# Optimization experiments

Hardware: AMD Instinct MI355X
Metric: run time of the kernel (lower is better)

The kernel has to match this reference:

```python
import jax, jax.numpy as jnp
import numpy as np

M, K, N = 32768, 2048, 2048  # tokens, in_features, out_features
QMIN, QMAX = -128, 127


def setup_inputs() -> dict:
    key = jax.random.key(0)
    ks = jax.random.split(key, 7)
    x = jax.random.normal(ks[0], (M, K), dtype=jnp.float32).astype(jnp.float16)
    int_weight = jax.random.randint(ks[1], (N, K), QMIN, QMAX + 1, dtype=jnp.int32).astype(jnp.int8)
    # calibrated-looking asymmetric activation quant params (fp16 buffers, [num_steps]=1)
    act_delta = (jax.random.uniform(ks[2], (1,), dtype=jnp.float32) * 0.02 + 0.005).astype(jnp.float16)
    act_zp = jnp.round(jax.random.normal(ks[3], (1,), dtype=jnp.float32) * 8.0).astype(jnp.float16)
    # per-output-channel weight scales; fuse precomputed dequant buffers consistently
    w_delta = jax.random.uniform(ks[4], (N,), dtype=jnp.float32) * 0.002 + 1e-4
    act_times_weight_delta = (act_delta.astype(jnp.float32) * w_delta)[None, :]  # [1, N]
    w_row_sum = jnp.sum(int_weight.astype(jnp.float32), axis=1)  # [N]
    zp_times_weight_channel_sum = (act_zp.astype(jnp.float32) * w_row_sum * act_times_weight_delta[0])[None, :]  # [1, N]
    bias = jax.random.normal(ks[5], (N,), dtype=jnp.float32) * 0.02
    return {
        "input": x,
        "act_delta": act_delta,
        "act_zp": act_zp,
        "zp_times_weight_channel_sum": zp_times_weight_channel_sum,
        "act_times_weight_delta": act_times_weight_delta,
        "bias": bias,
        "int_weight": int_weight,
    }


def reference(input, act_delta, act_zp, zp_times_weight_channel_sum,
              act_times_weight_delta, bias, int_weight):
    # current_step == num_steps - 1 == 0
    delta = act_delta[0].astype(jnp.float32)
    zp = act_zp[0].astype(jnp.float32)
    atwd = act_times_weight_delta[0]            # [N] = act_delta * weight_delta
    zp_sum = zp_times_weight_channel_sum[0]     # [N] = zp * rowsum(W_int) * atwd
    # asymmetric int8 activation quantization: q = clip(round(x/delta + zp))
    q = jnp.clip(jnp.round(input.astype(jnp.float32) / delta + zp), QMIN, QMAX).astype(jnp.int8)
    # int8 GEMM with int32 accumulation: [M,K] x [K,N]
    acc = jnp.matmul(q.astype(jnp.int32), int_weight.astype(jnp.int32).T)
    # fused dequant + zero-point correction + bias, cast to fp16
    out = acc.astype(jnp.float32) * atwd - zp_sum + bias
    return out.astype(jnp.float16)
```

## Files before the change

kernel.cpp:

```cpp
#include <hip/hip_runtime.h>
#include <hip/hip_fp16.h>
#include <stdint.h>

typedef int i32x4 __attribute__((ext_vector_type(4)));

#define BM 256
#define BN 256
#define BKB 64
#define NSLOT 4
#define SLOT_BYTES 32768
#define THREADS 512

__device__ __forceinline__ void gload_lds16(const void* g, void* l) {
  __builtin_amdgcn_global_load_lds(
      (const __attribute__((address_space(1))) unsigned int*)g,
      (__attribute__((address_space(3))) unsigned int*)l, 16, 0, 0);
}

__global__ __launch_bounds__(256) void quant_x_kernel(
    const float* __restrict__ x, const float* __restrict__ deltap,
    const float* __restrict__ zpp, int8_t* __restrict__ q, int n16) {
  int i = blockIdx.x * blockDim.x + threadIdx.x;
  if (i >= n16) return;
  const float rdelta = 1.0f / deltap[0];
  const float zp = zpp[0];
  const float4* src = (const float4*)x + (size_t)i * 4;
  int packed[4];
#pragma unroll
  for (int g = 0; g < 4; ++g) {
    float4 v = src[g];
    float f0 = fminf(127.f, fmaxf(-128.f, rintf(fmaf(v.x, rdelta, zp))));
    float f1 = fminf(127.f, fmaxf(-128.f, rintf(fmaf(v.y, rdelta, zp))));
    float f2 = fminf(127.f, fmaxf(-128.f, rintf(fmaf(v.z, rdelta, zp))));
    float f3 = fminf(127.f, fmaxf(-128.f, rintf(fmaf(v.w, rdelta, zp))));
    int q0 = (int)f0 & 255, q1 = (int)f1 & 255, q2 = (int)f2 & 255, q3 = (int)f3 & 255;
    packed[g] = q0 | (q1 << 8) | (q2 << 16) | (q3 << 24);
  }
  ((int4*)q)[i] = make_int4(packed[0], packed[1], packed[2], packed[3]);
}

__global__ __launch_bounds__(256) void pack_w_kernel(
    const int* __restrict__ w, int8_t* __restrict__ wp, int n16) {
  int i = blockIdx.x * blockDim.x + threadIdx.x;
  if (i >= n16) return;
  const int4* src = (const int4*)w + (size_t)i * 4;
  int packed[4];
#pragma unroll
  for (int g = 0; g < 4; ++g) {
    int4 v = src[g];
    packed[g] = (v.x & 255) | ((v.y & 255) << 8) | ((v.z & 255) << 16) | ((v.w & 255) << 24);
  }
  ((int4*)wp)[i] = make_int4(packed[0], packed[1], packed[2], packed[3]);
}

__global__ __launch_bounds__(THREADS, 2) void gemm_i8_kernel(
    const int8_t* __restrict__ Aq, const int8_t* __restrict__ Bw,
    const float* __restrict__ atwd, const float* __restrict__ zpws,
    const float* __restrict__ bias, float* __restrict__ out,
    int Mc, int Nc, int Kc) {
  __shared__ int8_t lds[NSLOT * SLOT_BYTES];

  const int nwg = gridDim.x;
  int bid = blockIdx.x;
  if ((nwg & 7) == 0) bid = (bid & 7) * (nwg >> 3) + (bid >> 3);
  const int nbn = Nc / BN;
  const int bm = bid / nbn;
  const int bn = bid % nbn;

  const int tid = threadIdx.x;
  const size_t K = (size_t)Kc;
  const int NT = Kc / BKB;

  const int srow = tid >> 2;
  const int c_log = (tid & 3) ^ ((tid >> 3) & 3);
  const int8_t* gA = Aq + ((size_t)(bm * BM + srow)) * K + c_log * 16;
  const int8_t* gB = Bw + ((size_t)(bn * BN + srow)) * K + c_log * 16;
  const size_t half_off = (size_t)128 * K;
  int8_t* ldst = &lds[tid * 16];

  auto stageA = [&](int t, int h) {
    gload_lds16(gA + (size_t)h * half_off + (size_t)t * BKB,
                ldst + (t & 3) * SLOT_BYTES + h * 8192);
  };
  auto stageB = [&](int t, int h) {
    gload_lds16(gB + (size_t)h * half_off + (size_t)t * BKB,
                ldst + (t & 3) * SLOT_BYTES + 16384 + h * 8192);
  };

  const int lane = tid & 63;
  const int wave = tid >> 6;
  const int wr = wave >> 2;
  const int wc = wave & 3;
  const int fr = lane & 15;
  const int kc = lane >> 4;
  const int coff = (kc ^ ((fr >> 1) & 3)) << 4;
  const int aRow = wr * 128 + fr;
  const int bRow = wc * 64 + fr;

  i32x4 acc[8][4] = {};

  stageA(0, 0); stageA(0, 1); stageB(0, 0); stageB(0, 1);
  if (NT > 1) { stageA(1, 0); stageA(1, 1); stageB(1, 0); stageB(1, 1); }
  if (NT > 2) { stageA(2, 0); stageA(2, 1); stageB(2, 0); stageB(2, 1); }
  if (NT >= 3) asm volatile("s_waitcnt vmcnt(8)" ::: "memory");
  else         asm volatile("s_waitcnt vmcnt(0)" ::: "memory");
  __builtin_amdgcn_s_barrier();

  for (int t = 0; t < NT; ++t) {
    const int8_t* sA = &lds[(t & 3) * SLOT_BYTES];
    const int8_t* sB = sA + 16384;
    const bool pf = (t + 3 < NT);
    i32x4 bfr[4], afr[4];

#pragma unroll
    for (int j = 0; j < 4; ++j)
      bfr[j] = *(const i32x4*)&sB[(bRow + j * 16) * 64 + coff];
#pragma unroll
    for (int i = 0; i < 4; ++i)
      afr[i] = *(const i32x4*)&sA[(aRow + i * 16) * 64 + coff];
    if (pf) { stageA(t + 3, 0); stageA(t + 3, 1); }
    __builtin_amdgcn_s_barrier();
    asm volatile("s_waitcnt lgkmcnt(0)" ::: "memory");
    __builtin_amdgcn_s_setprio(1);
#pragma unroll
    for (int i = 0; i < 4; ++i)
#pragma unroll
      for (int j = 0; j < 4; ++j)
        acc[i][j] = __builtin_amdgcn_mfma_i32_16x16x64_i8(afr[i], bfr[j], acc[i][j], 0, 0, 0);
    __builtin_amdgcn_s_setprio(0);
    __builtin_amdgcn_s_barrier();

#pragma unroll
    for (int i = 0; i < 4; ++i)
      afr[i] = *(const i32x4*)&sA[(aRow + 64 + i * 16) * 64 + coff];
    if (pf) { stageB(t + 3, 0); stageB(t + 3, 1); }
    __builtin_amdgcn_s_barrier();
    asm volatile("s_waitcnt lgkmcnt(0)" ::: "memory");
    __builtin_amdgcn_s_setprio(1);
#pragma unroll
    for (int i = 0; i < 4; ++i)
#pragma unroll
      for (int j = 0; j < 4; ++j)
        acc[4 + i][j] = __builtin_amdgcn_mfma_i32_16x16x64_i8(afr[i], bfr[j], acc[4 + i][j], 0, 0, 0);
    __builtin_amdgcn_s_setprio(0);
    if (t < NT - 3)       asm volatile("s_waitcnt vmcnt(8)" ::: "memory");
    else if (t == NT - 3) asm volatile("s_waitcnt vmcnt(4)" ::: "memory");
    else if (t == NT - 2) asm volatile("s_waitcnt vmcnt(0)" ::: "memory");
    __builtin_amdgcn_s_barrier();
  }

  const int r4 = (lane >> 4) << 2;
#pragma unroll
  for (int j = 0; j < 4; ++j) {
    const int cn = bn * BN + wc * 64 + j * 16 + fr;
    const float aw = atwd[cn];
    const float zs = zpws[cn];
    const float bs = bias[cn];
#pragma unroll
    for (int mi = 0; mi < 8; ++mi) {
      const size_t rbase = (size_t)(bm * BM + wr * 128 + mi * 16 + r4) * (size_t)Nc;
#pragma unroll
      for (int r = 0; r < 4; ++r) {
        float v = (float)acc[mi][j][r] * aw - zs + bs;
        v = __half2float(__float2half(v));
        out[rbase + (size_t)r * Nc + cn] = v;
      }
    }
  }
}

extern "C" void kernel_launch(void* const* d_in, const int* in_sizes, int n_in,
                              void* d_out, int out_size, void* d_ws, size_t ws_size,
                              hipStream_t stream) {
  const float* x         = (const float*)d_in[0];
  const float* act_delta = (const float*)d_in[1];
  const float* act_zp    = (const float*)d_in[2];
  const float* zpws      = (const float*)d_in[3];
  const float* atwd      = (const float*)d_in[4];
  const float* bias      = (const float*)d_in[5];
  const int*   w32       = (const int*)d_in[6];
  float* out = (float*)d_out;

  const int N = in_sizes[5];
  const int K = in_sizes[6] / N;
  const int M = in_sizes[0] / K;

  int8_t* q  = (int8_t*)d_ws;
  int8_t* wp = q + (size_t)M * K;

  {
    int n16 = (M * K) / 16;
    quant_x_kernel<<<(n16 + 255) / 256, 256, 0, stream>>>(x, act_delta, act_zp, q, n16);
  }
  {
    int n16 = (N * K) / 16;
    pack_w_kernel<<<(n16 + 255) / 256, 256, 0, stream>>>(w32, wp, n16);
  }
  {
    dim3 grid((M / BM) * (N / BN));
    gemm_i8_kernel<<<grid, THREADS, 0, stream>>>(q, wp, atwd, zpws, bias, out, M, N, K);
  }
}
```

Before: 271.1 us.

## Switch GEMM to BK=128 double-buffered LDS pipeline and grid-stride quantizer

Restructures the int8 GEMM main loop from a 4-slot, BK=64 ring with a prefetch depth of three tiles into a 2-slot, BK=128 double buffer. Each 64-wide K half of the next tile is prefetched in pieces interleaved with the four MFMA phases. This halves the number of outer iterations and amortizes barriers over more MFMA work, but prefetches only one tile ahead, so global-load latency may be less well hidden. The activation quantization kernel also becomes a grid-stride loop capped at 2048 blocks, which cuts block launch overhead.

```diff
diff --git a/kernel.cpp b/kernel.cpp
--- a/kernel.cpp
+++ b/kernel.cpp
@@ -6,10 +6,9 @@
 
 #define BM 256
 #define BN 256
-#define BKB 64
-#define NSLOT 4
-#define SLOT_BYTES 32768
+#define BK 128
 #define THREADS 512
+#define SLOT 65536
 
 __device__ __forceinline__ void gload_lds16(const void* g, void* l) {
   __builtin_amdgcn_global_load_lds(
@@ -20,23 +19,24 @@
 __global__ __launch_bounds__(256) void quant_x_kernel(
     const float* __restrict__ x, const float* __restrict__ deltap,
     const float* __restrict__ zpp, int8_t* __restrict__ q, int n16) {
-  int i = blockIdx.x * blockDim.x + threadIdx.x;
-  if (i >= n16) return;
   const float rdelta = 1.0f / deltap[0];
   const float zp = zpp[0];
-  const float4* src = (const float4*)x + (size_t)i * 4;
-  int packed[4];
-#pragma unroll
-  for (int g = 0; g < 4; ++g) {
-    float4 v = src[g];
-    float f0 = fminf(127.f, fmaxf(-128.f, rintf(fmaf(v.x, rdelta, zp))));
-    float f1 = fminf(127.f, fmaxf(-128.f, rintf(fmaf(v.y, rdelta, zp))));
-    float f2 = fminf(127.f, fmaxf(-128.f, rintf(fmaf(v.z, rdelta, zp))));
-    float f3 = fminf(127.f, fmaxf(-128.f, rintf(fmaf(v.w, rdelta, zp))));
-    int q0 = (int)f0 & 255, q1 = (int)f1 & 255, q2 = (int)f2 & 255, q3 = (int)f3 & 255;
-    packed[g] = q0 | (q1 << 8) | (q2 << 16) | (q3 << 24);
-  }
-  ((int4*)q)[i] = make_int4(packed[0], packed[1], packed[2], packed[3]);
+  for (int i = blockIdx.x * blockDim.x + threadIdx.x; i < n16;
+       i += gridDim.x * blockDim.x) {
+    const float4* src = (const float4*)x + (size_t)i * 4;
+    int packed[4];
+#pragma unroll
+    for (int g = 0; g < 4; ++g) {
+      float4 v = src[g];
+      float f0 = fminf(127.f, fmaxf(-128.f, rintf(fmaf(v.x, rdelta, zp))));
+      float f1 = fminf(127.f, fmaxf(-128.f, rintf(fmaf(v.y, rdelta, zp))));
+      float f2 = fminf(127.f, fmaxf(-128.f, rintf(fmaf(v.z, rdelta, zp))));
+      float f3 = fminf(127.f, fmaxf(-128.f, rintf(fmaf(v.w, rdelta, zp))));
+      int q0 = (int)f0 & 255, q1 = (int)f1 & 255, q2 = (int)f2 & 255, q3 = (int)f3 & 255;
+      packed[g] = q0 | (q1 << 8) | (q2 << 16) | (q3 << 24);
+    }
+    ((int4*)q)[i] = make_int4(packed[0], packed[1], packed[2], packed[3]);
+  }
 }
 
 __global__ __launch_bounds__(256) void pack_w_kernel(
@@ -58,7 +58,7 @@
     const float* __restrict__ atwd, const float* __restrict__ zpws,
     const float* __restrict__ bias, float* __restrict__ out,
     int Mc, int Nc, int Kc) {
-  __shared__ int8_t lds[NSLOT * SLOT_BYTES];
+  __shared__ int8_t lds[2 * SLOT];
 
   const int nwg = gridDim.x;
   int bid = blockIdx.x;
@@ -69,22 +69,21 @@
 
   const int tid = threadIdx.x;
   const size_t K = (size_t)Kc;
-  const int NT = Kc / BKB;
+  const int NT = Kc / BK;
 
   const int srow = tid >> 2;
-  const int c_log = (tid & 3) ^ ((tid >> 3) & 3);
-  const int8_t* gA = Aq + ((size_t)(bm * BM + srow)) * K + c_log * 16;
-  const int8_t* gB = Bw + ((size_t)(bn * BN + srow)) * K + c_log * 16;
-  const size_t half_off = (size_t)128 * K;
-  int8_t* ldst = &lds[tid * 16];
-
-  auto stageA = [&](int t, int h) {
-    gload_lds16(gA + (size_t)h * half_off + (size_t)t * BKB,
-                ldst + (t & 3) * SLOT_BYTES + h * 8192);
-  };
-  auto stageB = [&](int t, int h) {
-    gload_lds16(gB + (size_t)h * half_off + (size_t)t * BKB,
-                ldst + (t & 3) * SLOT_BYTES + 16384 + h * 8192);
+  const int lc = (tid & 3) ^ ((tid >> 3) & 3);
+  const int8_t* gA = Aq + ((size_t)(bm * BM + srow)) * K + lc * 16;
+  const int8_t* gB = Bw + ((size_t)(bn * BN + srow)) * K + lc * 16;
+  int8_t* lbase = &lds[tid * 16];
+  const size_t row128 = (size_t)128 * K;
+
+  auto stage = [&](int tt, int kh, int ab) {
+    const int8_t* g = ab ? gB : gA;
+    int8_t* l = lbase + (tt & 1) * SLOT + ab * 32768 + kh * 16384;
+    const size_t koff = (size_t)tt * BK + (size_t)kh * 64;
+    gload_lds16(g + koff, l);
+    gload_lds16(g + koff + row128, l + 8192);
   };
 
   const int lane = tid & 63;
@@ -93,60 +92,65 @@
   const int wc = wave & 3;
   const int fr = lane & 15;
   const int kc = lane >> 4;
-  const int coff = (kc ^ ((fr >> 1) & 3)) << 4;
+  const int coff = ((kc ^ ((fr >> 1) & 3)) << 4);
   const int aRow = wr * 128 + fr;
   const int bRow = wc * 64 + fr;
 
   i32x4 acc[8][4] = {};
-
-  stageA(0, 0); stageA(0, 1); stageB(0, 0); stageB(0, 1);
-  if (NT > 1) { stageA(1, 0); stageA(1, 1); stageB(1, 0); stageB(1, 1); }
-  if (NT > 2) { stageA(2, 0); stageA(2, 1); stageB(2, 0); stageB(2, 1); }
-  if (NT >= 3) asm volatile("s_waitcnt vmcnt(8)" ::: "memory");
-  else         asm volatile("s_waitcnt vmcnt(0)" ::: "memory");
-  __builtin_amdgcn_s_barrier();
+  i32x4 afr[4], bfr[4];
+
+#define READ_B(sb, kh)                                                        \
+  _Pragma("unroll")                                                           \
+  for (int j = 0; j < 4; ++j)                                                 \
+    bfr[j] = *(const i32x4*)&lds[(sb) + 32768 + (kh)*16384 +                  \
+                                 (bRow + j * 16) * 64 + coff];
+#define READ_A(sb, mh, kh)                                                    \
+  _Pragma("unroll")                                                           \
+  for (int i = 0; i < 4; ++i)                                                 \
+    afr[i] = *(const i32x4*)&lds[(sb) + (kh)*16384 +                          \
+                                 (aRow + (mh)*64 + i * 16) * 64 + coff];
+#define MFMA16(mh)                                                            \
+  __builtin_amdgcn_s_setprio(1);                                             \
+  _Pragma("unroll")                                                           \
+  for (int i = 0; i < 4; ++i)                                                 \
+    _Pragma("unroll")                                                         \
+    for (int j = 0; j < 4; ++j)                                               \
+      acc[(mh)*4 + i][j] =                                                    \
+          __builtin_amdgcn_mfma_i32_16x16x64_i8(afr[i], bfr[j],               \
+                                                acc[(mh)*4 + i][j], 0, 0, 0); \
+  __builtin_amdgcn_s_setprio(0);
+#define BAR __builtin_amdgcn_s_barrier()
+#define LGKM0 asm volatile("s_waitcnt lgkmcnt(0)" ::: "memory")
+
+  stage(0, 0, 0); stage(0, 0, 1);
+  stage(0, 1, 0); stage(0, 1, 1);
+  asm volatile("s_waitcnt vmcnt(4)" ::: "memory");
+  BAR;
 
   for (int t = 0; t < NT; ++t) {
-    const int8_t* sA = &lds[(t & 3) * SLOT_BYTES];
-    const int8_t* sB = sA + 16384;
-    const bool pf = (t + 3 < NT);
-    i32x4 bfr[4], afr[4];
-
-#pragma unroll
-    for (int j = 0; j < 4; ++j)
-      bfr[j] = *(const i32x4*)&sB[(bRow + j * 16) * 64 + coff];
-#pragma unroll
-    for (int i = 0; i < 4; ++i)
-      afr[i] = *(const i32x4*)&sA[(aRow + i * 16) * 64 + coff];
-    if (pf) { stageA(t + 3, 0); stageA(t + 3, 1); }
-    __builtin_amdgcn_s_barrier();
-    asm volatile("s_waitcnt lgkmcnt(0)" ::: "memory");
-    __builtin_amdgcn_s_setprio(1);
-#pragma unroll
-    for (int i = 0; i < 4; ++i)
-#pragma unroll
-      for (int j = 0; j < 4; ++j)
-        acc[i][j] = __builtin_amdgcn_mfma_i32_16x16x64_i8(afr[i], bfr[j], acc[i][j], 0, 0, 0);
-    __builtin_amdgcn_s_setprio(0);
-    __builtin_amdgcn_s_barrier();
-
-#pragma unroll
-    for (int i = 0; i < 4; ++i)
-      afr[i] = *(const i32x4*)&sA[(aRow + 64 + i * 16) * 64 + coff];
-    if (pf) { stageB(t + 3, 0); stageB(t + 3, 1); }
-    __builtin_amdgcn_s_barrier();
-    asm volatile("s_waitcnt lgkmcnt(0)" ::: "memory");
-    __builtin_amdgcn_s_setprio(1);
-#pragma unroll
-    for (int i = 0; i < 4; ++i)
-#pragma unroll
-      for (int j = 0; j < 4; ++j)
-        acc[4 + i][j] = __builtin_amdgcn_mfma_i32_16x16x64_i8(afr[i], bfr[j], acc[4 + i][j], 0, 0, 0);
-    __builtin_amdgcn_s_setprio(0);
-    if (t < NT - 3)       asm volatile("s_waitcnt vmcnt(8)" ::: "memory");
-    else if (t == NT - 3) asm volatile("s_waitcnt vmcnt(4)" ::: "memory");
-    else if (t == NT - 2) asm volatile("s_waitcnt vmcnt(0)" ::: "memory");
-    __builtin_amdgcn_s_barrier();
+    const int sb = (t & 1) * SLOT;
+    const bool pf = (t + 1 < NT);
+
+    READ_B(sb, 0); READ_A(sb, 0, 0);
+    if (pf) stage(t + 1, 0, 0);
+    BAR; LGKM0; MFMA16(0); BAR;
+
+    READ_A(sb, 1, 0);
+    if (pf) stage(t + 1, 0, 1);
+    BAR; LGKM0; MFMA16(1);
+    if (pf) asm volatile("s_waitcnt vmcnt(4)" ::: "memory");
+    else    asm volatile("s_waitcnt vmcnt(0)" ::: "memory");
+    BAR;
+
+    READ_B(sb, 1); READ_A(sb, 0, 1);
+    if (pf) stage(t + 1, 1, 0);
+    BAR; LGKM0; MFMA16(0); BAR;
+
+    READ_A(sb, 1, 1);
+    if (pf) stage(t + 1, 1, 1);
+    BAR; LGKM0; MFMA16(1);
+    if (pf) asm volatile("s_waitcnt vmcnt(4)" ::: "memory");
+    BAR;
   }
 
   const int r4 = (lane >> 4) << 2;
@@ -167,6 +171,11 @@
       }
     }
   }
+#undef READ_B
+#undef READ_A
+#undef MFMA16
+#undef BAR
+#undef LGKM0
 }
 
 extern "C" void kernel_launch(void* const* d_in, const int* in_sizes, int n_in,
@@ -190,7 +199,9 @@
 
   {
     int n16 = (M * K) / 16;
-    quant_x_kernel<<<(n16 + 255) / 256, 256, 0, stream>>>(x, act_delta, act_zp, q, n16);
+    int grid = (n16 + 255) / 256;
+    if (grid > 2048) grid = 2048;
+    quant_x_kernel<<<grid, 256, 0, stream>>>(x, act_delta, act_zp, q, n16);
   }
   {
     int n16 = (N * K) / 16;
```

Measured after the change: 272.1 us. About the same (+0.4%).

## Restructure GEMM main loop to one barrier per K-step and grid-stride quantization

Applied to the files above, without the earlier changes.

The GEMM inner loop now loads all A and B fragments for a K-step up front, issues the prefetch for step t+3 for both operands together, and runs both MFMA halves back-to-back. This drops the mid-iteration barriers, lgkmcnt waits and priority toggles, leaving one barrier per step (skipped on the last step) with sched_barrier fences. The point is to cut synchronisation overhead and let LDS reads overlap MFMA work, at the cost of higher register pressure from holding twice as many A fragments. The quant kernel becomes grid-stride with a capped grid, and the epilogue reorders its stores by row and hoists the per-column parameter loads.

```diff
diff --git a/kernel.cpp b/kernel.cpp
--- a/kernel.cpp
+++ b/kernel.cpp
@@ -20,23 +20,24 @@
 __global__ __launch_bounds__(256) void quant_x_kernel(
     const float* __restrict__ x, const float* __restrict__ deltap,
     const float* __restrict__ zpp, int8_t* __restrict__ q, int n16) {
-  int i = blockIdx.x * blockDim.x + threadIdx.x;
-  if (i >= n16) return;
   const float rdelta = 1.0f / deltap[0];
   const float zp = zpp[0];
-  const float4* src = (const float4*)x + (size_t)i * 4;
-  int packed[4];
-#pragma unroll
-  for (int g = 0; g < 4; ++g) {
-    float4 v = src[g];
-    float f0 = fminf(127.f, fmaxf(-128.f, rintf(fmaf(v.x, rdelta, zp))));
-    float f1 = fminf(127.f, fmaxf(-128.f, rintf(fmaf(v.y, rdelta, zp))));
-    float f2 = fminf(127.f, fmaxf(-128.f, rintf(fmaf(v.z, rdelta, zp))));
-    float f3 = fminf(127.f, fmaxf(-128.f, rintf(fmaf(v.w, rdelta, zp))));
-    int q0 = (int)f0 & 255, q1 = (int)f1 & 255, q2 = (int)f2 & 255, q3 = (int)f3 & 255;
-    packed[g] = q0 | (q1 << 8) | (q2 << 16) | (q3 << 24);
-  }
-  ((int4*)q)[i] = make_int4(packed[0], packed[1], packed[2], packed[3]);
+  for (int i = blockIdx.x * blockDim.x + threadIdx.x; i < n16;
+       i += gridDim.x * blockDim.x) {
+    const float4* src = (const float4*)x + (size_t)i * 4;
+    int packed[4];
+#pragma unroll
+    for (int g = 0; g < 4; ++g) {
+      float4 v = src[g];
+      float f0 = fminf(127.f, fmaxf(-128.f, rintf(fmaf(v.x, rdelta, zp))));
+      float f1 = fminf(127.f, fmaxf(-128.f, rintf(fmaf(v.y, rdelta, zp))));
+      float f2 = fminf(127.f, fmaxf(-128.f, rintf(fmaf(v.z, rdelta, zp))));
+      float f3 = fminf(127.f, fmaxf(-128.f, rintf(fmaf(v.w, rdelta, zp))));
+      int q0 = (int)f0 & 255, q1 = (int)f1 & 255, q2 = (int)f2 & 255, q3 = (int)f3 & 255;
+      packed[g] = q0 | (q1 << 8) | (q2 << 16) | (q3 << 24);
+    }
+    ((int4*)q)[i] = make_int4(packed[0], packed[1], packed[2], packed[3]);
+  }
 }
 
 __global__ __launch_bounds__(256) void pack_w_kernel(
@@ -72,19 +73,21 @@
   const int NT = Kc / BKB;
 
   const int srow = tid >> 2;
-  const int c_log = (tid & 3) ^ ((tid >> 3) & 3);
-  const int8_t* gA = Aq + ((size_t)(bm * BM + srow)) * K + c_log * 16;
-  const int8_t* gB = Bw + ((size_t)(bn * BN + srow)) * K + c_log * 16;
+  const int lc = (tid & 3) ^ ((tid >> 3) & 3);
+  const int8_t* gA = Aq + ((size_t)(bm * BM + srow)) * K + lc * 16;
+  const int8_t* gB = Bw + ((size_t)(bn * BN + srow)) * K + lc * 16;
   const size_t half_off = (size_t)128 * K;
   int8_t* ldst = &lds[tid * 16];
 
-  auto stageA = [&](int t, int h) {
-    gload_lds16(gA + (size_t)h * half_off + (size_t)t * BKB,
-                ldst + (t & 3) * SLOT_BYTES + h * 8192);
+  auto stageA = [&](int t) {
+    int8_t* l = ldst + (t & 3) * SLOT_BYTES;
+    gload_lds16(gA + (size_t)t * BKB, l);
+    gload_lds16(gA + (size_t)t * BKB + half_off, l + 8192);
   };
-  auto stageB = [&](int t, int h) {
-    gload_lds16(gB + (size_t)h * half_off + (size_t)t * BKB,
-                ldst + (t & 3) * SLOT_BYTES + 16384 + h * 8192);
+  auto stageB = [&](int t) {
+    int8_t* l = ldst + (t & 3) * SLOT_BYTES + 16384;
+    gload_lds16(gB + (size_t)t * BKB, l);
+    gload_lds16(gB + (size_t)t * BKB + half_off, l + 8192);
   };
 
   const int lane = tid & 63;
@@ -93,77 +96,77 @@
   const int wc = wave & 3;
   const int fr = lane & 15;
   const int kc = lane >> 4;
-  const int coff = (kc ^ ((fr >> 1) & 3)) << 4;
+  const int coff = ((kc ^ ((fr >> 1) & 3)) << 4);
   const int aRow = wr * 128 + fr;
   const int bRow = wc * 64 + fr;
 
   i32x4 acc[8][4] = {};
 
-  stageA(0, 0); stageA(0, 1); stageB(0, 0); stageB(0, 1);
-  if (NT > 1) { stageA(1, 0); stageA(1, 1); stageB(1, 0); stageB(1, 1); }
-  if (NT > 2) { stageA(2, 0); stageA(2, 1); stageB(2, 0); stageB(2, 1); }
-  if (NT >= 3) asm volatile("s_waitcnt vmcnt(8)" ::: "memory");
-  else         asm volatile("s_waitcnt vmcnt(0)" ::: "memory");
+  stageA(0); stageB(0);
+  if (NT > 1) { stageA(1); stageB(1); }
+  if (NT > 2) { stageA(2); stageB(2); }
+  if (NT > 2)      asm volatile("s_waitcnt vmcnt(8)" ::: "memory");
+  else if (NT > 1) asm volatile("s_waitcnt vmcnt(4)" ::: "memory");
+  else             asm volatile("s_waitcnt vmcnt(0)" ::: "memory");
   __builtin_amdgcn_s_barrier();
+  __builtin_amdgcn_sched_barrier(0);
 
   for (int t = 0; t < NT; ++t) {
     const int8_t* sA = &lds[(t & 3) * SLOT_BYTES];
     const int8_t* sB = sA + 16384;
-    const bool pf = (t + 3 < NT);
-    i32x4 bfr[4], afr[4];
-
+
+    i32x4 bfr[4], a0[4], a1[4];
 #pragma unroll
     for (int j = 0; j < 4; ++j)
       bfr[j] = *(const i32x4*)&sB[(bRow + j * 16) * 64 + coff];
 #pragma unroll
     for (int i = 0; i < 4; ++i)
-      afr[i] = *(const i32x4*)&sA[(aRow + i * 16) * 64 + coff];
-    if (pf) { stageA(t + 3, 0); stageA(t + 3, 1); }
-    __builtin_amdgcn_s_barrier();
-    asm volatile("s_waitcnt lgkmcnt(0)" ::: "memory");
-    __builtin_amdgcn_s_setprio(1);
+      a0[i] = *(const i32x4*)&sA[(aRow + i * 16) * 64 + coff];
+#pragma unroll
+    for (int i = 0; i < 4; ++i)
+      a1[i] = *(const i32x4*)&sA[(aRow + 64 + i * 16) * 64 + coff];
+
+    if (t + 3 < NT) { stageA(t + 3); stageB(t + 3); }
+
 #pragma unroll
     for (int i = 0; i < 4; ++i)
 #pragma unroll
       for (int j = 0; j < 4; ++j)
-        acc[i][j] = __builtin_amdgcn_mfma_i32_16x16x64_i8(afr[i], bfr[j], acc[i][j], 0, 0, 0);
-    __builtin_amdgcn_s_setprio(0);
-    __builtin_amdgcn_s_barrier();
-
-#pragma unroll
-    for (int i = 0; i < 4; ++i)
-      afr[i] = *(const i32x4*)&sA[(aRow + 64 + i * 16) * 64 + coff];
-    if (pf) { stageB(t + 3, 0); stageB(t + 3, 1); }
-    __builtin_amdgcn_s_barrier();
-    asm volatile("s_waitcnt lgkmcnt(0)" ::: "memory");
-    __builtin_amdgcn_s_setprio(1);
+        acc[i][j] = __builtin_amdgcn_mfma_i32_16x16x64_i8(a0[i], bfr[j], acc[i][j], 0, 0, 0);
 #pragma unroll
     for (int i = 0; i < 4; ++i)
 #pragma unroll
       for (int j = 0; j < 4; ++j)
-        acc[4 + i][j] = __builtin_amdgcn_mfma_i32_16x16x64_i8(afr[i], bfr[j], acc[4 + i][j], 0, 0, 0);
-    __builtin_amdgcn_s_setprio(0);
-    if (t < NT - 3)       asm volatile("s_waitcnt vmcnt(8)" ::: "memory");
-    else if (t == NT - 3) asm volatile("s_waitcnt vmcnt(4)" ::: "memory");
-    else if (t == NT - 2) asm volatile("s_waitcnt vmcnt(0)" ::: "memory");
-    __builtin_amdgcn_s_barrier();
+        acc[4 + i][j] = __builtin_amdgcn_mfma_i32_16x16x64_i8(a1[i], bfr[j], acc[4 + i][j], 0, 0, 0);
+
+    if (t < NT - 1) {
+      if (t + 3 < NT)       asm volatile("s_waitcnt vmcnt(8)" ::: "memory");
+      else if (t + 3 == NT) asm volatile("s_waitcnt vmcnt(4)" ::: "memory");
+      else                  asm volatile("s_waitcnt vmcnt(0)" ::: "memory");
+      __builtin_amdgcn_s_barrier();
+      __builtin_amdgcn_sched_barrier(0);
+    }
   }
 
   const int r4 = (lane >> 4) << 2;
+  const int cn0 = bn * BN + wc * 64 + fr;
+  float aw4[4], zs4[4], bs4[4];
 #pragma unroll
   for (int j = 0; j < 4; ++j) {
-    const int cn = bn * BN + wc * 64 + j * 16 + fr;
-    const float aw = atwd[cn];
-    const float zs = zpws[cn];
-    const float bs = bias[cn];
-#pragma unroll
-    for (int mi = 0; mi < 8; ++mi) {
-      const size_t rbase = (size_t)(bm * BM + wr * 128 + mi * 16 + r4) * (size_t)Nc;
-#pragma unroll
-      for (int r = 0; r < 4; ++r) {
-        float v = (float)acc[mi][j][r] * aw - zs + bs;
+    aw4[j] = atwd[cn0 + j * 16];
+    zs4[j] = zpws[cn0 + j * 16];
+    bs4[j] = bias[cn0 + j * 16];
+  }
+#pragma unroll
+  for (int mi = 0; mi < 8; ++mi) {
+#pragma unroll
+    for (int r = 0; r < 4; ++r) {
+      const size_t rbase = (size_t)(bm * BM + wr * 128 + mi * 16 + r4 + r) * (size_t)Nc;
+#pragma unroll
+      for (int j = 0; j < 4; ++j) {
+        float v = (float)acc[mi][j][r] * aw4[j] - zs4[j] + bs4[j];
         v = __half2float(__float2half(v));
-        out[rbase + (size_t)r * Nc + cn] = v;
+        out[rbase + cn0 + j * 16] = v;
       }
     }
   }
@@ -190,7 +193,9 @@
 
   {
     int n16 = (M * K) / 16;
-    quant_x_kernel<<<(n16 + 255) / 256, 256, 0, stream>>>(x, act_delta, act_zp, q, n16);
+    int grid = (n16 + 255) / 256;
+    if (grid > 2048) grid = 2048;
+    quant_x_kernel<<<grid, 256, 0, stream>>>(x, act_delta, act_zp, q, n16);
   }
   {
     int n16 = (N * K) / 16;
```

After: 252.5 us. 6.9% less time.
